# Kernel optimization log

Hardware: AMD Instinct MI355X
Metric: run time of the kernel (lower is better)

Reference implementation:

```python
import jax, jax.numpy as jnp
import numpy as np

N_NODES = 100000
N_EDGES = 3200000
D_IN = 256
D_OUT = 256


def setup_inputs() -> dict:
    key = jax.random.key(0)
    k1, k2, k3, k4, k5 = jax.random.split(key, 5)
    # kaiming-uniform-like init for weight
    bound = float(np.sqrt(6.0 / D_IN))
    weight = jax.random.uniform(k1, (D_IN, D_OUT), dtype=jnp.float32, minval=-bound, maxval=bound)
    bias = jnp.zeros((D_OUT,), dtype=jnp.float32)
    input_feature = jax.random.normal(k2, (N_NODES, D_IN), dtype=jnp.float32)
    # sparse_poly in COO form: (row, col, val), typical normalized graph polynomial values
    edge_row = jax.random.randint(k3, (N_EDGES,), 0, N_NODES, dtype=jnp.int32)
    edge_col = jax.random.randint(k4, (N_EDGES,), 0, N_NODES, dtype=jnp.int32)
    edge_val = jax.random.uniform(k5, (N_EDGES,), dtype=jnp.float32)
    return {
        "input_feature": input_feature,
        "weight": weight,
        "bias": bias,
        "edge_val": edge_val,
        "edge_row": edge_row,
        "edge_col": edge_col,
    }


def reference(input_feature, weight, bias, edge_val, edge_row, edge_col):
    # support = X @ W  -> [N, D_OUT]
    support = input_feature @ weight
    # output = sparse_poly @ support  (COO SpMM):
    # gather source rows, scale by edge values, scatter-add into destination rows
    messages = edge_val[:, None] * support[edge_col]  # [E, D_OUT]
    output = jax.ops.segment_sum(messages, edge_row, num_segments=N_NODES)
    return output + bias
```

## Files before the change

kernel.cpp:

```cpp
#include <hip/hip_runtime.h>

#define D 256
#define GBM 128
#define WT_PITCH 264
#define BSH 9
#define RPB 512
#define NBMAX 256
#define TILE 4096

using bf16x8 = __attribute__((ext_vector_type(8))) short;
using f32x4  = __attribute__((ext_vector_type(4))) float;

static __device__ __forceinline__ unsigned short f2bf(float f) {
    unsigned u = __builtin_bit_cast(unsigned, f);
    return (unsigned short)((u + 0x7fffu + ((u >> 16) & 1u)) >> 16);
}
static __device__ __forceinline__ float as_f(unsigned u) {
    return __builtin_bit_cast(float, u);
}

__global__ void wt_kernel(const float* __restrict__ W, unsigned short* __restrict__ Wt) {
    int idx = blockIdx.x * blockDim.x + threadIdx.x;
    int n = idx & 255, k = idx >> 8;
    Wt[n * 256 + k] = f2bf(W[k * 256 + n]);
}

__global__ __launch_bounds__(512) void gemm_mfma(const float* __restrict__ X,
                                                 const unsigned short* __restrict__ Wt,
                                                 unsigned short* __restrict__ S, int N) {
    __shared__ unsigned short wlds[256 * WT_PITCH];

    for (int c = threadIdx.x; c < 8192; c += 512) {
        int n = c >> 5, kc = c & 31;
        uint4 v = *reinterpret_cast<const uint4*>(Wt + n * 256 + kc * 8);
        *reinterpret_cast<uint4*>(&wlds[n * WT_PITCH + kc * 8]) = v;
    }
    __syncthreads();

    const int lane = threadIdx.x & 63;
    const int wave = threadIdx.x >> 6;
    const int row0 = blockIdx.x * GBM + wave * 16;
    const int l16  = lane & 15;
    const int kgrp = lane >> 4;
    const int arow = min(row0 + l16, N - 1);
    const float* xp = X + (size_t)arow * 256 + kgrp * 8;

    f32x4 acc[16];
#pragma unroll
    for (int i = 0; i < 16; i++) acc[i] = (f32x4)(0.0f);

#pragma unroll
    for (int ks = 0; ks < 8; ks++) {
        float4 a0 = *reinterpret_cast<const float4*>(xp + ks * 32);
        float4 a1 = *reinterpret_cast<const float4*>(xp + ks * 32 + 4);
        bf16x8 af;
        af[0] = (short)f2bf(a0.x); af[1] = (short)f2bf(a0.y);
        af[2] = (short)f2bf(a0.z); af[3] = (short)f2bf(a0.w);
        af[4] = (short)f2bf(a1.x); af[5] = (short)f2bf(a1.y);
        af[6] = (short)f2bf(a1.z); af[7] = (short)f2bf(a1.w);
#pragma unroll
        for (int nt = 0; nt < 16; nt++) {
            bf16x8 bf = *reinterpret_cast<const bf16x8*>(
                &wlds[(nt * 16 + l16) * WT_PITCH + ks * 32 + kgrp * 8]);
            acc[nt] = __builtin_amdgcn_mfma_f32_16x16x32_bf16(af, bf, acc[nt], 0, 0, 0);
        }
    }

#pragma unroll
    for (int nt = 0; nt < 16; nt++) {
#pragma unroll
        for (int j = 0; j < 4; j++) {
            int r = row0 + kgrp * 4 + j;
            if (r < N) S[(size_t)r * 256 + nt * 16 + l16] = f2bf(acc[nt][j]);
        }
    }
}

__global__ __launch_bounds__(256) void bucket_hist(const int* __restrict__ rows,
                                                   int* __restrict__ bcounts,
                                                   int E, int NB) {
    __shared__ int lh[NBMAX];
    for (int i = threadIdx.x; i < NB; i += 256) lh[i] = 0;
    __syncthreads();
    const int stride = gridDim.x * 256;
    for (int e = blockIdx.x * 256 + threadIdx.x; e < E; e += stride)
        atomicAdd(&lh[rows[e] >> BSH], 1);
    __syncthreads();
    for (int i = threadIdx.x; i < NB; i += 256) {
        int v = lh[i];
        if (v) atomicAdd(&bcounts[i], v);
    }
}

__global__ __launch_bounds__(1024) void bscan_kernel(const int* __restrict__ bcounts,
                                                     int* __restrict__ boffs,
                                                     int* __restrict__ bcursor, int NB) {
    __shared__ int wsum[16];
    const int t = threadIdx.x, lane = t & 63, w = t >> 6;
    int x = (t < NB) ? bcounts[t] : 0;
    int s = x;
#pragma unroll
    for (int d = 1; d < 64; d <<= 1) {
        int y = __shfl_up(s, d);
        if (lane >= d) s += y;
    }
    if (lane == 63) wsum[w] = s;
    __syncthreads();
    if (w == 0) {
        int ws = (lane < 16) ? wsum[lane] : 0;
#pragma unroll
        for (int d = 1; d < 16; d <<= 1) {
            int y = __shfl_up(ws, d);
            if (lane >= d) ws += y;
        }
        if (lane < 16) wsum[lane] = ws;
    }
    __syncthreads();
    int excl = (w ? wsum[w - 1] : 0) + s - x;
    if (t < NB) { boffs[t] = excl; bcursor[t] = excl; }
}

__global__ __launch_bounds__(256) void partition_kernel(const int* __restrict__ rows,
                                                        const int* __restrict__ cols,
                                                        const float* __restrict__ vals,
                                                        int* __restrict__ bcursor,
                                                        int2* __restrict__ packed,
                                                        int E, int NB) {
    __shared__ int lh[NBMAX];
    __shared__ int gbase[NBMAX];
    const int t = threadIdx.x;
    const int e0 = blockIdx.x * TILE;

    for (int i = t; i < NB; i += 256) lh[i] = 0;
    __syncthreads();

    int bk[16], rk[16], pc[16], pv[16];
#pragma unroll
    for (int j = 0; j < 16; j++) {
        int idx = e0 + j * 256 + t;
        if (idx < E) {
            int r = rows[idx];
            bk[j] = r >> BSH;
            rk[j] = atomicAdd(&lh[bk[j]], 1);
            pc[j] = ((r & (RPB - 1)) << 17) | cols[idx];
            pv[j] = __float_as_int(vals[idx]);
        } else {
            bk[j] = -1;
        }
    }
    __syncthreads();

    for (int i = t; i < NB; i += 256) {
        int c = lh[i];
        gbase[i] = c ? atomicAdd(&bcursor[i], c) : 0;
    }
    __syncthreads();

#pragma unroll
    for (int j = 0; j < 16; j++) {
        if (bk[j] >= 0) {
            int2 p; p.x = pc[j]; p.y = pv[j];
            packed[(size_t)gbase[bk[j]] + rk[j]] = p;
        }
    }
}

__global__ __launch_bounds__(256) void bucket_scatter(const int2* __restrict__ packed,
                                                      const int* __restrict__ boffs,
                                                      const int* __restrict__ bcounts,
                                                      int* __restrict__ offs,
                                                      int* __restrict__ counts,
                                                      int2* __restrict__ cv, int N) {
    __shared__ int cnt[RPB];
    __shared__ int lofs[RPB];
    __shared__ int wsum[4];
    const int b = blockIdx.x, t = threadIdx.x;
    const int base = boffs[b], nb = bcounts[b];

    for (int i = t; i < RPB; i += 256) cnt[i] = 0;
    __syncthreads();
    for (int i = t; i < nb; i += 256)
        atomicAdd(&cnt[((unsigned)packed[base + i].x) >> 17], 1);
    __syncthreads();

    const int lane = t & 63, w = t >> 6;
    int a0 = cnt[2 * t], a1 = cnt[2 * t + 1];
    int s = a0 + a1;
    int ss = s;
#pragma unroll
    for (int d = 1; d < 64; d <<= 1) {
        int y = __shfl_up(ss, d);
        if (lane >= d) ss += y;
    }
    if (lane == 63) wsum[w] = ss;
    __syncthreads();
    int wex = 0;
    if (w > 0) wex += wsum[0];
    if (w > 1) wex += wsum[1];
    if (w > 2) wex += wsum[2];
    int excl = wex + ss - s;

    const int r0 = b << BSH;
    int r = r0 + 2 * t;
    if (r < N)     { offs[r]     = base + excl;      counts[r]     = a0; }
    if (r + 1 < N) { offs[r + 1] = base + excl + a0; counts[r + 1] = a1; }
    lofs[2 * t]     = excl;
    lofs[2 * t + 1] = excl + a0;
    __syncthreads();

    for (int i = t; i < nb; i += 256) {
        int2 p = packed[base + i];
        int lr = ((unsigned)p.x) >> 17;
        int pos = base + atomicAdd(&lofs[lr], 1);
        int2 o;
        o.x = p.x & 0x1FFFF;
        o.y = p.y;
        cv[pos] = o;
    }
}

__global__ __launch_bounds__(256) void spmm_kernel(const unsigned short* __restrict__ S,
                                                   const int* __restrict__ offs,
                                                   const int* __restrict__ counts,
                                                   const int2* __restrict__ cv,
                                                   const float* __restrict__ bias,
                                                   float* __restrict__ out, int N) {
    const int lane = threadIdx.x & 63;
    const int r = blockIdx.x * 4 + (threadIdx.x >> 6);
    if (r >= N) return;
    const char* Sb = reinterpret_cast<const char*>(S);

    float4 acc = { 0.f, 0.f, 0.f, 0.f };
    int i = offs[r];
    const int end = i + counts[r];

#define GATHER(c, v)                                                              \
    {                                                                             \
        uint2 sv = *reinterpret_cast<const uint2*>(Sb + ((size_t)(c) << 9) + (lane << 3)); \
        acc.x += (v) * as_f(sv.x << 16);                                          \
        acc.y += (v) * as_f(sv.x & 0xffff0000u);                                  \
        acc.z += (v) * as_f(sv.y << 16);                                          \
        acc.w += (v) * as_f(sv.y & 0xffff0000u);                                  \
    }

    for (; i + 3 < end; i += 4) {
        int2 e0 = cv[i], e1 = cv[i + 1], e2 = cv[i + 2], e3 = cv[i + 3];
        GATHER(e0.x, as_f((unsigned)e0.y));
        GATHER(e1.x, as_f((unsigned)e1.y));
        GATHER(e2.x, as_f((unsigned)e2.y));
        GATHER(e3.x, as_f((unsigned)e3.y));
    }
    for (; i < end; i++) {
        int2 e0 = cv[i];
        GATHER(e0.x, as_f((unsigned)e0.y));
    }
#undef GATHER

    float4 b = reinterpret_cast<const float4*>(bias)[lane];
    float4 o = { acc.x + b.x, acc.y + b.y, acc.z + b.z, acc.w + b.w };
    reinterpret_cast<float4*>(out)[(size_t)r * 64 + lane] = o;
}

extern "C" void kernel_launch(void* const* d_in, const int* in_sizes, int n_in,
                              void* d_out, int out_size, void* d_ws, size_t ws_size,
                              hipStream_t stream) {
    const float* X     = (const float*)d_in[0];
    const float* W     = (const float*)d_in[1];
    const float* bias  = (const float*)d_in[2];
    const float* evals = (const float*)d_in[3];
    const int*   erow  = (const int*)d_in[4];
    const int*   ecol  = (const int*)d_in[5];
    float* out = (float*)d_out;

    const int N = in_sizes[0] / D;
    const int E = in_sizes[3];
    const int NB = (N + RPB - 1) >> BSH;

    char* ws = (char*)d_ws;
    size_t off = 0;
    auto alloc = [&](size_t bytes) {
        void* p = ws + off;
        off += (bytes + 255) & ~(size_t)255;
        return p;
    };
    unsigned short* S  = (unsigned short*)alloc((size_t)N * D * sizeof(unsigned short));
    unsigned short* Wt = (unsigned short*)alloc((size_t)D * D * sizeof(unsigned short));
    int* bcounts = (int*)alloc((size_t)NB * sizeof(int));
    int* boffs   = (int*)alloc((size_t)NB * sizeof(int));
    int* bcursor = (int*)alloc((size_t)NB * sizeof(int));
    int* offs    = (int*)alloc((size_t)N * sizeof(int));
    int* counts  = (int*)alloc((size_t)N * sizeof(int));
    int2* packed = (int2*)alloc((size_t)E * sizeof(int2));
    int2* cv     = (int2*)alloc((size_t)E * sizeof(int2));

    wt_kernel<<<(D * D) / 256, 256, 0, stream>>>(W, Wt);
    gemm_mfma<<<(N + GBM - 1) / GBM, 512, 0, stream>>>(X, Wt, S, N);
    hipMemsetAsync(bcounts, 0, (size_t)NB * sizeof(int), stream);
    bucket_hist<<<1024, 256, 0, stream>>>(erow, bcounts, E, NB);
    bscan_kernel<<<1, 1024, 0, stream>>>(bcounts, boffs, bcursor, NB);
    partition_kernel<<<(E + TILE - 1) / TILE, 256, 0, stream>>>(erow, ecol, evals, bcursor,
                                                                packed, E, NB);
    bucket_scatter<<<NB, 256, 0, stream>>>(packed, boffs, bcounts, offs, counts, cv, N);
    spmm_kernel<<<(N + 3) / 4, 256, 0, stream>>>(S, offs, counts, cv, bias, out, N);
}
```

Measured before the change: 413.2 us.

## Sort edges by column tile per row and sweep SpMM over column tiles

The bucket scatter now sorts each row's edges by a coarse column-tile key (column >> 12), so every row's neighbours come out ordered by source tile. The SpMM kernel has each wave own 16 rows and step through the column tiles in lockstep, so gathers from the bf16 support matrix stay within a smaller working set that may fit in cache. This adds per-edge break checks, divergent while-loops and a larger LDS histogram. The GEMM is also changed to 256-row blocks with 1024 threads, and buckets now cover 256 rows instead of 512.

Result: slower. 718.3 us (+73.8%).

```diff
diff --git a/kernel.cpp b/kernel.cpp
--- a/kernel.cpp
+++ b/kernel.cpp
@@ -1,12 +1,14 @@
 #include <hip/hip_runtime.h>
 
 #define D 256
-#define GBM 128
+#define GBM 256
 #define WT_PITCH 264
-#define BSH 9
-#define RPB 512
-#define NBMAX 256
+#define BSH 8
+#define RPB 256
+#define NBMAX 512
 #define TILE 4096
+#define CTSH 12
+#define NKEY (RPB * 32)
 
 using bf16x8 = __attribute__((ext_vector_type(8))) short;
 using f32x4  = __attribute__((ext_vector_type(4))) float;
@@ -25,12 +27,12 @@
     Wt[n * 256 + k] = f2bf(W[k * 256 + n]);
 }
 
-__global__ __launch_bounds__(512) void gemm_mfma(const float* __restrict__ X,
-                                                 const unsigned short* __restrict__ Wt,
-                                                 unsigned short* __restrict__ S, int N) {
+__global__ __launch_bounds__(1024) void gemm_mfma(const float* __restrict__ X,
+                                                  const unsigned short* __restrict__ Wt,
+                                                  unsigned short* __restrict__ S, int N) {
     __shared__ unsigned short wlds[256 * WT_PITCH];
 
-    for (int c = threadIdx.x; c < 8192; c += 512) {
+    for (int c = threadIdx.x; c < 8192; c += 1024) {
         int n = c >> 5, kc = c & 31;
         uint4 v = *reinterpret_cast<const uint4*>(Wt + n * 256 + kc * 8);
         *reinterpret_cast<uint4*>(&wlds[n * WT_PITCH + kc * 8]) = v;
@@ -171,22 +173,26 @@
                                                       int* __restrict__ offs,
                                                       int* __restrict__ counts,
                                                       int2* __restrict__ cv, int N) {
-    __shared__ int cnt[RPB];
-    __shared__ int lofs[RPB];
+    __shared__ int cnt[NKEY];
     __shared__ int wsum[4];
     const int b = blockIdx.x, t = threadIdx.x;
     const int base = boffs[b], nb = bcounts[b];
-
-    for (int i = t; i < RPB; i += 256) cnt[i] = 0;
-    __syncthreads();
-    for (int i = t; i < nb; i += 256)
-        atomicAdd(&cnt[((unsigned)packed[base + i].x) >> 17], 1);
-    __syncthreads();
-
     const int lane = t & 63, w = t >> 6;
-    int a0 = cnt[2 * t], a1 = cnt[2 * t + 1];
-    int s = a0 + a1;
-    int ss = s;
+
+    for (int i = t; i < NKEY; i += 256) cnt[i] = 0;
+    __syncthreads();
+    for (int i = t; i < nb; i += 256) {
+        int px = packed[base + i].x;
+        int key = ((((unsigned)px) >> 17) << 5) | ((px & 0x1FFFF) >> CTSH);
+        atomicAdd(&cnt[key], 1);
+    }
+    __syncthreads();
+
+    const int K = NKEY / 256;
+    int tsum = 0;
+#pragma unroll
+    for (int k = 0; k < K; k++) tsum += cnt[t * K + k];
+    int ss = tsum;
 #pragma unroll
     for (int d = 1; d < 64; d <<= 1) {
         int y = __shfl_up(ss, d);
@@ -198,20 +204,32 @@
     if (w > 0) wex += wsum[0];
     if (w > 1) wex += wsum[1];
     if (w > 2) wex += wsum[2];
-    int excl = wex + ss - s;
+    int run = wex + ss - tsum;
+    __syncthreads();
+#pragma unroll
+    for (int k = 0; k < K; k++) {
+        int c = cnt[t * K + k];
+        cnt[t * K + k] = run;
+        run += c;
+    }
+    __syncthreads();
 
     const int r0 = b << BSH;
-    int r = r0 + 2 * t;
-    if (r < N)     { offs[r]     = base + excl;      counts[r]     = a0; }
-    if (r + 1 < N) { offs[r + 1] = base + excl + a0; counts[r + 1] = a1; }
-    lofs[2 * t]     = excl;
-    lofs[2 * t + 1] = excl + a0;
+    for (int lr = t; lr < RPB; lr += 256) {
+        int r = r0 + lr;
+        if (r < N) {
+            int s0 = cnt[lr << 5];
+            int s1 = (lr == RPB - 1) ? nb : cnt[(lr + 1) << 5];
+            offs[r] = base + s0;
+            counts[r] = s1 - s0;
+        }
+    }
     __syncthreads();
 
     for (int i = t; i < nb; i += 256) {
         int2 p = packed[base + i];
-        int lr = ((unsigned)p.x) >> 17;
-        int pos = base + atomicAdd(&lofs[lr], 1);
+        int key = ((((unsigned)p.x) >> 17) << 5) | ((p.x & 0x1FFFF) >> CTSH);
+        int pos = base + atomicAdd(&cnt[key], 1);
         int2 o;
         o.x = p.x & 0x1FFFF;
         o.y = p.y;
@@ -224,41 +242,58 @@
                                                    const int* __restrict__ counts,
                                                    const int2* __restrict__ cv,
                                                    const float* __restrict__ bias,
-                                                   float* __restrict__ out, int N) {
+                                                   float* __restrict__ out,
+                                                   int N, int nct) {
     const int lane = threadIdx.x & 63;
-    const int r = blockIdx.x * 4 + (threadIdx.x >> 6);
-    if (r >= N) return;
+    const int wave = __builtin_amdgcn_readfirstlane(threadIdx.x >> 6);
+    const int r0 = blockIdx.x * 64 + wave * 16;
     const char* Sb = reinterpret_cast<const char*>(S);
 
-    float4 acc = { 0.f, 0.f, 0.f, 0.f };
-    int i = offs[r];
-    const int end = i + counts[r];
-
-#define GATHER(c, v)                                                              \
+    float4 acc[16];
+    int ip[16], ep[16];
+#pragma unroll
+    for (int g = 0; g < 16; g++) {
+        acc[g] = make_float4(0.f, 0.f, 0.f, 0.f);
+        int r = r0 + g;
+        if (r < N) { ip[g] = offs[r]; ep[g] = ip[g] + counts[r]; }
+        else       { ip[g] = 0; ep[g] = 0; }
+    }
+
+#define GATHER(c, v, A)                                                           \
     {                                                                             \
         uint2 sv = *reinterpret_cast<const uint2*>(Sb + ((size_t)(c) << 9) + (lane << 3)); \
-        acc.x += (v) * as_f(sv.x << 16);                                          \
-        acc.y += (v) * as_f(sv.x & 0xffff0000u);                                  \
-        acc.z += (v) * as_f(sv.y << 16);                                          \
-        acc.w += (v) * as_f(sv.y & 0xffff0000u);                                  \
-    }
-
-    for (; i + 3 < end; i += 4) {
-        int2 e0 = cv[i], e1 = cv[i + 1], e2 = cv[i + 2], e3 = cv[i + 3];
-        GATHER(e0.x, as_f((unsigned)e0.y));
-        GATHER(e1.x, as_f((unsigned)e1.y));
-        GATHER(e2.x, as_f((unsigned)e2.y));
-        GATHER(e3.x, as_f((unsigned)e3.y));
-    }
-    for (; i < end; i++) {
-        int2 e0 = cv[i];
-        GATHER(e0.x, as_f((unsigned)e0.y));
+        A.x += (v) * as_f(sv.x << 16);                                            \
+        A.y += (v) * as_f(sv.x & 0xffff0000u);                                    \
+        A.z += (v) * as_f(sv.y << 16);                                            \
+        A.w += (v) * as_f(sv.y & 0xffff0000u);                                    \
+    }
+
+    for (int ct = 0; ct < nct; ct++) {
+        const int bound = (ct + 1) << CTSH;
+#pragma unroll
+        for (int g = 0; g < 16; g++) {
+            int i = ip[g];
+            const int e = ep[g];
+            while (i < e) {
+                int2 p = cv[i];
+                if (p.x >= bound) break;
+                GATHER(p.x, as_f((unsigned)p.y), acc[g]);
+                i++;
+            }
+            ip[g] = i;
+        }
     }
 #undef GATHER
 
     float4 b = reinterpret_cast<const float4*>(bias)[lane];
-    float4 o = { acc.x + b.x, acc.y + b.y, acc.z + b.z, acc.w + b.w };
-    reinterpret_cast<float4*>(out)[(size_t)r * 64 + lane] = o;
+#pragma unroll
+    for (int g = 0; g < 16; g++) {
+        int r = r0 + g;
+        if (r < N) {
+            float4 o = { acc[g].x + b.x, acc[g].y + b.y, acc[g].z + b.z, acc[g].w + b.w };
+            reinterpret_cast<float4*>(out)[(size_t)r * 64 + lane] = o;
+        }
+    }
 }
 
 extern "C" void kernel_launch(void* const* d_in, const int* in_sizes, int n_in,
@@ -275,6 +310,7 @@
     const int N = in_sizes[0] / D;
     const int E = in_sizes[3];
     const int NB = (N + RPB - 1) >> BSH;
+    const int nct = ((N - 1) >> CTSH) + 1;
 
     char* ws = (char*)d_ws;
     size_t off = 0;
@@ -294,12 +330,12 @@
     int2* cv     = (int2*)alloc((size_t)E * sizeof(int2));
 
     wt_kernel<<<(D * D) / 256, 256, 0, stream>>>(W, Wt);
-    gemm_mfma<<<(N + GBM - 1) / GBM, 512, 0, stream>>>(X, Wt, S, N);
+    gemm_mfma<<<(N + GBM - 1) / GBM, 1024, 0, stream>>>(X, Wt, S, N);
     hipMemsetAsync(bcounts, 0, (size_t)NB * sizeof(int), stream);
     bucket_hist<<<1024, 256, 0, stream>>>(erow, bcounts, E, NB);
     bscan_kernel<<<1, 1024, 0, stream>>>(bcounts, boffs, bcursor, NB);
     partition_kernel<<<(E + TILE - 1) / TILE, 256, 0, stream>>>(erow, ecol, evals, bcursor,
                                                                 packed, E, NB);
     bucket_scatter<<<NB, 256, 0, stream>>>(packed, boffs, bcounts, offs, counts, cv, N);
-    spmm_kernel<<<(N + 3) / 4, 256, 0, stream>>>(S, offs, counts, cv, bias, out, N);
-}
+    spmm_kernel<<<(N + 63) / 64, 256, 0, stream>>>(S, offs, counts, cv, bias, out, N, nct);
+}
```

## Gather two edges per wave in SpMM, fold memset, enlarge GEMM blocks

Applied to the files above, without the earlier changes.

The SpMM kernel now splits each wave into two 32-lane halves. Each half gathers a different edge's bf16 row with 16-byte loads, and the halves are combined with a cross-half shuffle before the bias add and store. This aims to widen memory transactions and raise memory-level parallelism on the gather-bound step. The bucket-count memset is folded into the weight-transpose kernel to save a launch. The GEMM block grows to 1024 threads covering 256 rows, which amortises the shared-memory weight load but may reduce occupancy.

Measured after the change: 391.0 us. 1.06x faster.

```diff
diff --git a/kernel.cpp b/kernel.cpp
--- a/kernel.cpp
+++ b/kernel.cpp
@@ -1,7 +1,7 @@
 #include <hip/hip_runtime.h>
 
 #define D 256
-#define GBM 128
+#define GBM 256
 #define WT_PITCH 264
 #define BSH 9
 #define RPB 512
@@ -19,18 +19,20 @@
     return __builtin_bit_cast(float, u);
 }
 
-__global__ void wt_kernel(const float* __restrict__ W, unsigned short* __restrict__ Wt) {
+__global__ void wt_kernel(const float* __restrict__ W, unsigned short* __restrict__ Wt,
+                          int* __restrict__ bcounts, int NB) {
     int idx = blockIdx.x * blockDim.x + threadIdx.x;
     int n = idx & 255, k = idx >> 8;
     Wt[n * 256 + k] = f2bf(W[k * 256 + n]);
-}
-
-__global__ __launch_bounds__(512) void gemm_mfma(const float* __restrict__ X,
-                                                 const unsigned short* __restrict__ Wt,
-                                                 unsigned short* __restrict__ S, int N) {
+    if (blockIdx.x == 0 && threadIdx.x < NB) bcounts[threadIdx.x] = 0;
+}
+
+__global__ __launch_bounds__(1024) void gemm_mfma(const float* __restrict__ X,
+                                                  const unsigned short* __restrict__ Wt,
+                                                  unsigned short* __restrict__ S, int N) {
     __shared__ unsigned short wlds[256 * WT_PITCH];
 
-    for (int c = threadIdx.x; c < 8192; c += 512) {
+    for (int c = threadIdx.x; c < 8192; c += 1024) {
         int n = c >> 5, kc = c & 31;
         uint4 v = *reinterpret_cast<const uint4*>(Wt + n * 256 + kc * 8);
         *reinterpret_cast<uint4*>(&wlds[n * WT_PITCH + kc * 8]) = v;
@@ -176,6 +178,7 @@
     __shared__ int wsum[4];
     const int b = blockIdx.x, t = threadIdx.x;
     const int base = boffs[b], nb = bcounts[b];
+    const int lane = t & 63, w = t >> 6;
 
     for (int i = t; i < RPB; i += 256) cnt[i] = 0;
     __syncthreads();
@@ -183,7 +186,6 @@
         atomicAdd(&cnt[((unsigned)packed[base + i].x) >> 17], 1);
     __syncthreads();
 
-    const int lane = t & 63, w = t >> 6;
     int a0 = cnt[2 * t], a1 = cnt[2 * t + 1];
     int s = a0 + a1;
     int ss = s;
@@ -226,39 +228,56 @@
                                                    const float* __restrict__ bias,
                                                    float* __restrict__ out, int N) {
     const int lane = threadIdx.x & 63;
+    const int half = lane >> 5;
+    const int l32  = lane & 31;
     const int r = blockIdx.x * 4 + (threadIdx.x >> 6);
     if (r >= N) return;
     const char* Sb = reinterpret_cast<const char*>(S);
 
-    float4 acc = { 0.f, 0.f, 0.f, 0.f };
+    float acc[8] = {0.f, 0.f, 0.f, 0.f, 0.f, 0.f, 0.f, 0.f};
     int i = offs[r];
     const int end = i + counts[r];
 
-#define GATHER(c, v)                                                              \
+#define GPAIR(c0, v0, c1, v1)                                                     \
     {                                                                             \
-        uint2 sv = *reinterpret_cast<const uint2*>(Sb + ((size_t)(c) << 9) + (lane << 3)); \
-        acc.x += (v) * as_f(sv.x << 16);                                          \
-        acc.y += (v) * as_f(sv.x & 0xffff0000u);                                  \
-        acc.z += (v) * as_f(sv.y << 16);                                          \
-        acc.w += (v) * as_f(sv.y & 0xffff0000u);                                  \
-    }
-
-    for (; i + 3 < end; i += 4) {
-        int2 e0 = cv[i], e1 = cv[i + 1], e2 = cv[i + 2], e3 = cv[i + 3];
-        GATHER(e0.x, as_f((unsigned)e0.y));
-        GATHER(e1.x, as_f((unsigned)e1.y));
-        GATHER(e2.x, as_f((unsigned)e2.y));
-        GATHER(e3.x, as_f((unsigned)e3.y));
-    }
-    for (; i < end; i++) {
+        int   c = half ? (c1) : (c0);                                             \
+        float v = half ? (v1) : (v0);                                             \
+        uint4 sv = *reinterpret_cast<const uint4*>(Sb + ((size_t)c << 9) + (l32 << 4)); \
+        acc[0] += v * as_f(sv.x << 16);                                           \
+        acc[1] += v * as_f(sv.x & 0xffff0000u);                                   \
+        acc[2] += v * as_f(sv.y << 16);                                           \
+        acc[3] += v * as_f(sv.y & 0xffff0000u);                                   \
+        acc[4] += v * as_f(sv.z << 16);                                           \
+        acc[5] += v * as_f(sv.z & 0xffff0000u);                                   \
+        acc[6] += v * as_f(sv.w << 16);                                           \
+        acc[7] += v * as_f(sv.w & 0xffff0000u);                                   \
+    }
+
+    for (; i + 7 < end; i += 8) {
+        int2 e0 = cv[i],     e1 = cv[i + 1], e2 = cv[i + 2], e3 = cv[i + 3];
+        int2 e4 = cv[i + 4], e5 = cv[i + 5], e6 = cv[i + 6], e7 = cv[i + 7];
+        GPAIR(e0.x, as_f((unsigned)e0.y), e1.x, as_f((unsigned)e1.y));
+        GPAIR(e2.x, as_f((unsigned)e2.y), e3.x, as_f((unsigned)e3.y));
+        GPAIR(e4.x, as_f((unsigned)e4.y), e5.x, as_f((unsigned)e5.y));
+        GPAIR(e6.x, as_f((unsigned)e6.y), e7.x, as_f((unsigned)e7.y));
+    }
+    for (; i + 1 < end; i += 2) {
+        int2 e0 = cv[i], e1 = cv[i + 1];
+        GPAIR(e0.x, as_f((unsigned)e0.y), e1.x, as_f((unsigned)e1.y));
+    }
+    if (i < end) {
         int2 e0 = cv[i];
-        GATHER(e0.x, as_f((unsigned)e0.y));
-    }
-#undef GATHER
-
-    float4 b = reinterpret_cast<const float4*>(bias)[lane];
-    float4 o = { acc.x + b.x, acc.y + b.y, acc.z + b.z, acc.w + b.w };
-    reinterpret_cast<float4*>(out)[(size_t)r * 64 + lane] = o;
+        GPAIR(e0.x, as_f((unsigned)e0.y), e0.x, 0.0f);
+    }
+#undef GPAIR
+
+#pragma unroll
+    for (int j = 0; j < 8; j++) acc[j] += __shfl_xor(acc[j], 32);
+
+    float4 bv = reinterpret_cast<const float4*>(bias)[l32 * 2 + half];
+    float4 o = { acc[half * 4 + 0] + bv.x, acc[half * 4 + 1] + bv.y,
+                 acc[half * 4 + 2] + bv.z, acc[half * 4 + 3] + bv.w };
+    reinterpret_cast<float4*>(out)[(size_t)r * 64 + l32 * 2 + half] = o;
 }
 
 extern "C" void kernel_launch(void* const* d_in, const int* in_sizes, int n_in,
@@ -274,7 +293,7 @@
 
     const int N = in_sizes[0] / D;
     const int E = in_sizes[3];
-    const int NB = (N + RPB - 1) >> BSH;
+    const int NB = ((N + RPB - 1) >> BSH);
 
     char* ws = (char*)d_ws;
     size_t off = 0;
@@ -293,9 +312,8 @@
     int2* packed = (int2*)alloc((size_t)E * sizeof(int2));
     int2* cv     = (int2*)alloc((size_t)E * sizeof(int2));
 
-    wt_kernel<<<(D * D) / 256, 256, 0, stream>>>(W, Wt);
-    gemm_mfma<<<(N + GBM - 1) / GBM, 512, 0, stream>>>(X, Wt, S, N);
-    hipMemsetAsync(bcounts, 0, (size_t)NB * sizeof(int), stream);
+    wt_kernel<<<(D * D) / 256, 256, 0, stream>>>(W, Wt, bcounts, NB);
+    gemm_mfma<<<(N + GBM - 1) / GBM, 1024, 0, stream>>>(X, Wt, S, N);
     bucket_hist<<<1024, 256, 0, stream>>>(erow, bcounts, E, NB);
     bscan_kernel<<<1, 1024, 0, stream>>>(bcounts, boffs, bcursor, NB);
     partition_kernel<<<(E + TILE - 1) / TILE, 256, 0, stream>>>(erow, ecol, evals, bcursor,
```
